# Optimization experiments

Hardware: AMD Instinct MI355X
Metric: run time of the kernel (lower is better)

Reference implementation:

```python
import jax, jax.numpy as jnp
import numpy as np

N, F, D, M, B, K = 100000, 256, 128, 10, 32768, 32


def setup_inputs() -> dict:
    key = jax.random.key(0)
    ks = jax.random.split(key, 14)
    stdv = float(1.0 / np.sqrt(D))
    inp = {
        "feature": jax.random.normal(ks[0], (N, F), jnp.float32),
        "flow_char_adj": jax.random.uniform(ks[1], (M, N), jnp.float32),
        "history": jax.random.randint(ks[2], (B, K), 0, N),
        "item_id": jax.random.randint(ks[3], (B,), 0, N),
        "category_r": jax.random.randint(ks[4], (B,), 0, 2),
        "category_n": jax.random.randint(ks[5], (B,), 0, 2),
        "PA_level": jax.random.randint(ks[6], (B,), 0, M),
        # learned parameters (uniform(-stdv, stdv) as in reset_parameters)
        "weight_emb": jax.random.uniform(ks[7], (F, D), jnp.float32, -stdv, stdv),
        "bias_emb": jax.random.uniform(ks[8], (D,), jnp.float32, -stdv, stdv),
        "weight_character": jax.random.uniform(ks[9], (2 * D, D), jnp.float32, -stdv, stdv),
        "att1_w": jax.random.uniform(ks[10], (D, 1), jnp.float32, -stdv, stdv),
        "att1_b": jax.random.uniform(ks[11], (1,), jnp.float32, -stdv, stdv),
        "linear1_w": jax.random.uniform(ks[12], (2 * D, D), jnp.float32, -stdv, stdv),
        "linear1_b": jax.random.uniform(ks[13], (D,), jnp.float32, -stdv, stdv),
    }
    return inp


def reference(feature, flow_char_adj, weight_emb, bias_emb, weight_character,
              att1_w, att1_b, linear1_w, linear1_b,
              history, item_id, category_r, category_n, PA_level):
    # embedding_encode
    flow_emb = feature @ weight_emb + bias_emb              # [N, D]
    character_emb = flow_char_adj @ flow_emb                # [M, D] (spmm)

    # character_modeling (shared for r and n)
    def char_lat(cat, pa):
        ce = jnp.concatenate([character_emb[cat], character_emb[pa]], axis=1)  # [B, 2D]
        return jax.nn.sigmoid(ce @ weight_character)        # [B, D]

    lat_r = char_lat(category_r, PA_level)
    lat_n = char_lat(category_n, PA_level)

    # attribute_agg: mix flow emb with its 2 category embeddings
    flow_all = (flow_emb + flow_char_adj[:2].T @ character_emb[:2]) * 0.5  # [N, D]

    # Flow_Aggregator: per-node neighbor attention (batched over ragged lists,
    # here padded to fixed degree K)
    neigh = flow_all[history]                                # [B, K, D]
    scores = neigh @ att1_w + att1_b                         # [B, K, 1]
    att = jax.nn.softmax(scores, axis=1)                     # softmax over neighbors
    agg = jnp.sum(att * neigh, axis=1)                       # [B, D]

    # NOTE: in the torch source, self_flow_latent is mutated in-place so
    # self_feats aliases neigh_feats -> both halves of the concat equal agg.
    combined = jnp.concatenate([agg, agg], axis=1)           # [B, 2D]
    out = jax.nn.relu(combined @ linear1_w + linear1_b)      # [B, D] (dropout p=0)

    pred_r = jnp.sum(lat_r * out, axis=1)                    # [B]
    pred_n = jnp.sum(lat_n * out, axis=1)                    # [B]
    return pred_r, pred_n
```

## Files before the change

### kernel.cpp

```cpp
#include <hip/hip_runtime.h>
#include <cmath>

#define NN 100000
#define FF 256
#define DDIM 128
#define MM 10
#define BB 32768
#define KK 32
#define NB1 1563

#define OFF_Q    0
#define OFF_CE   100096
#define OFF_LAT  101376
#define OFF_WPP  103936
#define OFF_CE01 120320
#define OFF_CS   120576
#define OFF_AGG  120592
#define OFF_FE8  4314896
#define OFF_WF   7514896

typedef __attribute__((ext_vector_type(8))) short bf16x8;
typedef __attribute__((ext_vector_type(4))) float floatx4;
typedef __attribute__((ext_vector_type(2))) float floatx2;

__device__ __forceinline__ unsigned short f2bf(float x) {
  union { float f; unsigned u; } v; v.f = x;
  unsigned r = v.u + 0x7FFFu + ((v.u >> 16) & 1u);
  return (unsigned short)(r >> 16);
}
__device__ __forceinline__ float bf2f(unsigned short h) {
  union { float f; unsigned u; } v; v.u = ((unsigned)h) << 16;
  return v.f;
}

__global__ __launch_bounds__(256) void k0_wprep(const float* __restrict__ wemb,
                                                short* __restrict__ wf)
{
  const int t = blockIdx.x * 256 + threadIdx.x;
  const int kk = t >> 9, rem = t & 511;
  const int ct = rem >> 6, l = rem & 63;
  const int n = ct * 16 + (l & 15);
  const int kbase = kk * 32 + (l >> 4) * 8;
  short hi[8], lo[8];
#pragma unroll
  for (int j = 0; j < 8; j++) {
    const float x = wemb[(kbase + j) * 128 + n];
    const unsigned short h = f2bf(x);
    hi[j] = (short)h;
    lo[j] = (short)f2bf(x - bf2f(h));
  }
  const int off = ((kk * 8 + ct) * 64 + l) * 8;
  *reinterpret_cast<int4*>(&wf[off])         = *reinterpret_cast<int4*>(hi);
  *reinterpret_cast<int4*>(&wf[32768 + off]) = *reinterpret_cast<int4*>(lo);
}

__device__ __forceinline__ void split8v(float4 a, float4 b,
                                        bf16x8& hi8, bf16x8& lo8)
{
  const float xs[8] = {a.x, a.y, a.z, a.w, b.x, b.y, b.z, b.w};
  short h[8], l[8];
#pragma unroll
  for (int j = 0; j < 8; j++) {
    const unsigned short hh = f2bf(xs[j]);
    h[j] = (short)hh;
    l[j] = (short)f2bf(xs[j] - bf2f(hh));
  }
  hi8 = *reinterpret_cast<bf16x8*>(h);
  lo8 = *reinterpret_cast<bf16x8*>(l);
}

__global__ __launch_bounds__(128) void k1_fused(const float* __restrict__ feat,
    const short* __restrict__ wf, const float* __restrict__ bemb,
    const float* __restrict__ attw, const float* __restrict__ adj,
    float* __restrict__ q, unsigned char* __restrict__ fe8,
    float* __restrict__ ce)
{
  __shared__ __align__(16) unsigned char ldst[128 * 144];
  const int tid = threadIdx.x;
  const int wv = tid >> 6, l = tid & 63;
  const int lane16 = l & 15, quad = l >> 4;
  const int rowbase = blockIdx.x * 64 + wv * 32;

  floatx4 acc[2][8];
#pragma unroll
  for (int rt = 0; rt < 2; rt++)
#pragma unroll
    for (int ct = 0; ct < 8; ct++) acc[rt][ct] = floatx4{0.f, 0.f, 0.f, 0.f};

  int r0 = rowbase + lane16;      if (r0 > NN - 1) r0 = NN - 1;
  int r1 = rowbase + 16 + lane16; if (r1 > NN - 1) r1 = NN - 1;
  const float* pa0 = &feat[(size_t)r0 * 256 + quad * 8];
  const float* pa1 = &feat[(size_t)r1 * 256 + quad * 8];

  float4 A0a = *reinterpret_cast<const float4*>(pa0);
  float4 A0b = *reinterpret_cast<const float4*>(pa0 + 4);
  float4 A1a = *reinterpret_cast<const float4*>(pa1);
  float4 A1b = *reinterpret_cast<const float4*>(pa1 + 4);

  for (int kk = 0; kk < 8; kk++) {
    float4 N0a, N0b, N1a, N1b;
    if (kk < 7) {
      N0a = *reinterpret_cast<const float4*>(pa0 + (kk + 1) * 32);
      N0b = *reinterpret_cast<const float4*>(pa0 + (kk + 1) * 32 + 4);
      N1a = *reinterpret_cast<const float4*>(pa1 + (kk + 1) * 32);
      N1b = *reinterpret_cast<const float4*>(pa1 + (kk + 1) * 32 + 4);
    }
    bf16x8 a0h, a0l, a1h, a1l;
    split8v(A0a, A0b, a0h, a0l);
    split8v(A1a, A1b, a1h, a1l);
    const short* wb = &wf[kk * 4096 + l * 8];
#pragma unroll
    for (int ct = 0; ct < 8; ct++) {
      const bf16x8 bh = *reinterpret_cast<const bf16x8*>(&wb[ct * 512]);
      const bf16x8 bl = *reinterpret_cast<const bf16x8*>(&wb[32768 + ct * 512]);
      acc[0][ct] = __builtin_amdgcn_mfma_f32_16x16x32_bf16(a0h, bh, acc[0][ct], 0, 0, 0);
      acc[1][ct] = __builtin_amdgcn_mfma_f32_16x16x32_bf16(a1h, bh, acc[1][ct], 0, 0, 0);
      acc[0][ct] = __builtin_amdgcn_mfma_f32_16x16x32_bf16(a0l, bh, acc[0][ct], 0, 0, 0);
      acc[1][ct] = __builtin_amdgcn_mfma_f32_16x16x32_bf16(a1l, bh, acc[1][ct], 0, 0, 0);
      acc[0][ct] = __builtin_amdgcn_mfma_f32_16x16x32_bf16(a0h, bl, acc[0][ct], 0, 0, 0);
      acc[1][ct] = __builtin_amdgcn_mfma_f32_16x16x32_bf16(a1h, bl, acc[1][ct], 0, 0, 0);
    }
    A0a = N0a; A0b = N0b; A1a = N1a; A1b = N1b;
  }

  float bembv[8], attwv[8];
#pragma unroll
  for (int ct = 0; ct < 8; ct++) {
    bembv[ct] = bemb[ct * 16 + lane16];
    attwv[ct] = attw[ct * 16 + lane16];
  }
#pragma unroll
  for (int rt = 0; rt < 2; rt++) {
#pragma unroll
    for (int reg = 0; reg < 4; reg++) {
      const int rloc = (rt * 16 + quad * 4 + reg) + wv * 32;
      const int r = blockIdx.x * 64 + rloc;
      float v[8]; float qp = 0.f;
#pragma unroll
      for (int ct = 0; ct < 8; ct++) {
        v[ct] = acc[rt][ct][reg] + bembv[ct];
        qp = fmaf(v[ct], attwv[ct], qp);
      }
      acc[rt][0][reg] = v[0]; acc[rt][1][reg] = v[1]; acc[rt][2][reg] = v[2]; acc[rt][3][reg] = v[3];
      acc[rt][4][reg] = v[4]; acc[rt][5][reg] = v[5]; acc[rt][6][reg] = v[6]; acc[rt][7][reg] = v[7];
      qp += __shfl_xor(qp, 1, 16);
      qp += __shfl_xor(qp, 2, 16);
      qp += __shfl_xor(qp, 4, 16);
      qp += __shfl_xor(qp, 8, 16);
      if (r < NN) {
        unsigned u0 = __builtin_amdgcn_cvt_pk_fp8_f32(v[0], v[1], 0, false);
        u0 = __builtin_amdgcn_cvt_pk_fp8_f32(v[2], v[3], u0, true);
        unsigned u1 = __builtin_amdgcn_cvt_pk_fp8_f32(v[4], v[5], 0, false);
        u1 = __builtin_amdgcn_cvt_pk_fp8_f32(v[6], v[7], u1, true);
        *reinterpret_cast<uint2*>(&fe8[(size_t)r * 128 + lane16 * 8]) = make_uint2(u0, u1);
        if (lane16 == 0) q[r] = 0.5f * qp;
      }
    }
  }
#pragma unroll
  for (int rt = 0; rt < 2; rt++) {
#pragma unroll
    for (int rp = 0; rp < 2; rp++) {
      const int rloc = wv * 32 + rt * 16 + quad * 4 + rp * 2;
      const int g0 = blockIdx.x * 64 + rloc;
#pragma unroll
      for (int ct = 0; ct < 8; ct++) {
        const unsigned short h0 = (g0     < NN) ? f2bf(acc[rt][ct][rp * 2])     : (unsigned short)0;
        const unsigned short h1 = (g0 + 1 < NN) ? f2bf(acc[rt][ct][rp * 2 + 1]) : (unsigned short)0;
        const unsigned pk = (unsigned)h0 | ((unsigned)h1 << 16);
        *reinterpret_cast<unsigned*>(&ldst[(ct * 16 + lane16) * 144 + rloc * 2]) = pk;
      }
    }
  }
  __syncthreads();

  floatx4 cacc[4];
#pragma unroll
  for (int tt = 0; tt < 4; tt++) cacc[tt] = floatx4{0.f, 0.f, 0.f, 0.f};
  const int mclamp = (lane16 < 10) ? lane16 : 9;
  for (int kc = 0; kc < 2; kc++) {
    int n0 = blockIdx.x * 64 + kc * 32 + quad * 8;
    if (n0 > NN - 8) n0 = NN - 8;
    const float4 f0 = *reinterpret_cast<const float4*>(&adj[(size_t)mclamp * NN + n0]);
    const float4 f1 = *reinterpret_cast<const float4*>(&adj[(size_t)mclamp * NN + n0 + 4]);
    short af[8];
    af[0] = (short)f2bf(f0.x); af[1] = (short)f2bf(f0.y);
    af[2] = (short)f2bf(f0.z); af[3] = (short)f2bf(f0.w);
    af[4] = (short)f2bf(f1.x); af[5] = (short)f2bf(f1.y);
    af[6] = (short)f2bf(f1.z); af[7] = (short)f2bf(f1.w);
    const bf16x8 afr = *reinterpret_cast<bf16x8*>(af);
#pragma unroll
    for (int tt = 0; tt < 4; tt++) {
      const int col = (wv * 4 + tt) * 16 + lane16;
      const bf16x8 bfr = *reinterpret_cast<const bf16x8*>(
          &ldst[col * 144 + (kc * 32 + quad * 8) * 2]);
      cacc[tt] = __builtin_amdgcn_mfma_f32_16x16x32_bf16(afr, bfr, cacc[tt], 0, 0, 0);
    }
  }
#pragma unroll
  for (int tt = 0; tt < 4; tt++) {
#pragma unroll
    for (int reg = 0; reg < 4; reg++) {
      const int m = quad * 4 + reg;
      if (m < 10)
        atomicAdd(&ce[m * 128 + (wv * 4 + tt) * 16 + lane16], cacc[tt][reg]);
    }
  }
}

template<int NCHUNK>
__device__ __forceinline__ void gemm_main(const float* __restrict__ A, int lda, int rowclamp,
                                          const float* __restrict__ W,
                                          int rowbase, int tid,
                                          float (*AT)[128], float (*WT)[128],
                                          float (&acc)[8][8])
{
  const int a_r  = tid >> 4;
  const int a_f4 = tid & 15;
  const int w_k  = tid >> 5;
  const int w_f4 = tid & 31;
  const int tx = tid & 15, ty = tid >> 4;

#pragma unroll
  for (int i = 0; i < 8; i++)
#pragma unroll
    for (int j = 0; j < 8; j++) acc[i][j] = 0.f;

  for (int cc = 0; cc < NCHUNK; cc++) {
    const int kc = cc * 64;
#pragma unroll
    for (int i = 0; i < 8; i++) {
      int r = a_r + 16 * i;
      int gr = rowbase + r; gr = (gr > rowclamp) ? rowclamp : gr;
      const float4 v = *reinterpret_cast<const float4*>(&A[gr * lda + kc + a_f4 * 4]);
      const int X = a_f4 * 4;
      const int col = r ^ X;
      AT[X + 0][col] = v.x;
      AT[X + 1][col] = v.y;
      AT[X + 2][col] = v.z;
      AT[X + 3][col] = v.w;
    }
#pragma unroll
    for (int i = 0; i < 8; i++) {
      const int k = w_k + 8 * i;
      *reinterpret_cast<float4*>(&WT[k][w_f4 * 4]) =
          *reinterpret_cast<const float4*>(&W[(kc + k) * 128 + w_f4 * 4]);
    }
    __syncthreads();
#pragma unroll 8
    for (int k = 0; k < 64; k++) {
      const int X = k & 60;
      const float4 va0 = *reinterpret_cast<const float4*>(&AT[k][(ty * 4) ^ X]);
      const float4 va1 = *reinterpret_cast<const float4*>(&AT[k][((ty * 4) ^ X) + 64]);
      const float4 vb0 = *reinterpret_cast<const float4*>(&WT[k][tx * 4]);
      const float4 vb1 = *reinterpret_cast<const float4*>(&WT[k][tx * 4 + 64]);
      const float a[8] = {va0.x, va0.y, va0.z, va0.w, va1.x, va1.y, va1.z, va1.w};
      const float b[8] = {vb0.x, vb0.y, vb0.z, vb0.w, vb1.x, vb1.y, vb1.z, vb1.w};
#pragma unroll
      for (int i = 0; i < 8; i++)
#pragma unroll
        for (int j = 0; j < 8; j++)
          acc[i][j] = fmaf(a[i], b[j], acc[i][j]);
    }
    __syncthreads();
  }
}

__global__ __launch_bounds__(128) void k3_prep(const float* __restrict__ ce,
    const float* __restrict__ wchar, const float* __restrict__ attw,
    const float* __restrict__ l1w,
    float* __restrict__ latTab, float* __restrict__ Wpp,
    float* __restrict__ ce01p, float* __restrict__ cs)
{
  const int blk = blockIdx.x, tid = threadIdx.x;
  __shared__ float cec[128], cep[128];
  if (blk < 20) {
    const int c = blk / 10, p = blk % 10;
    cec[tid] = ce[c * 128 + tid];
    cep[tid] = ce[p * 128 + tid];
    __syncthreads();
    float s = 0.f;
#pragma unroll 4
    for (int j = 0; j < 128; j++) {
      s = fmaf(cec[j], wchar[j * 128 + tid], s);
      s = fmaf(cep[j], wchar[(128 + j) * 128 + tid], s);
    }
    latTab[blk * 128 + tid] = 1.f / (1.f + expf(-s));
  } else {
    const float s0 = ce[tid];
    const float s1 = ce[128 + tid];
    const int pidx = (tid & 15) * 8 + (tid >> 4);
    ce01p[pidx] = s0;
    ce01p[128 + pidx] = s1;
    cec[tid] = s0 * attw[tid];
    cep[tid] = s1 * attw[tid];
    __syncthreads();
    if (tid < 64) {
      float p0 = cec[tid] + cec[tid + 64];
      float p1 = cep[tid] + cep[tid + 64];
#pragma unroll
      for (int off = 32; off >= 1; off >>= 1) {
        p0 += __shfl_xor(p0, off);
        p1 += __shfl_xor(p1, off);
      }
      if (tid == 0) { cs[0] = 0.5f * p0; cs[1] = 0.5f * p1; }
    }
    for (int i = 0; i < 128; i++) {
      const int pi = (i & 15) * 8 + (i >> 4);
      Wpp[pi * 128 + tid] = l1w[i * 128 + tid] + l1w[16384 + i * 128 + tid];
    }
  }
}

__global__ __launch_bounds__(256) void k4a_attn(const unsigned char* __restrict__ fe8,
    const float* __restrict__ q, const float* __restrict__ adj,
    const int* __restrict__ history, const float* __restrict__ cs,
    const float* __restrict__ attb_p, const float* __restrict__ ce01p,
    float* __restrict__ agg)
{
  const int tid = threadIdx.x;
  const int lane = tid & 63;
  const int wv = tid >> 6;
  const int half = lane >> 5;
  const int t = lane & 31;
  const int b = blockIdx.x * 8 + wv * 2 + half;

  const int n_my = history[b * 32 + t];
  const float a0 = adj[n_my];
  const float a1 = adj[NN + n_my];
  const float sc = q[n_my] + a0 * cs[0] + a1 * cs[1] + attb_p[0];
  float m = sc;
#pragma unroll
  for (int off = 16; off >= 1; off >>= 1) m = fmaxf(m, __shfl_xor(m, off, 32));
  const float e = expf(sc - m);
  float sum = e;
#pragma unroll
  for (int off = 16; off >= 1; off >>= 1) sum += __shfl_xor(sum, off, 32);
  const float att = e / sum;
  float p0 = att * a0, p1 = att * a1;
#pragma unroll
  for (int off = 16; off >= 1; off >>= 1) {
    p0 += __shfl_xor(p0, off, 32);
    p1 += __shfl_xor(p1, off, 32);
  }

  float4 acc = make_float4(0.f, 0.f, 0.f, 0.f);
#pragma unroll
  for (int k = 0; k < 32; k++) {
    const int nk = __shfl(n_my, k, 32);
    const float ak = __shfl(att, k, 32);
    const unsigned u = *reinterpret_cast<const unsigned*>(&fe8[(size_t)nk * 128 + t * 4]);
    const floatx2 lo = __builtin_amdgcn_cvt_pk_f32_fp8(u, false);
    const floatx2 hi = __builtin_amdgcn_cvt_pk_f32_fp8(u, true);
    acc.x = fmaf(ak, lo[0], acc.x);
    acc.y = fmaf(ak, lo[1], acc.y);
    acc.z = fmaf(ak, hi[0], acc.z);
    acc.w = fmaf(ak, hi[1], acc.w);
  }
  const int col = t * 4;
  const float4 c0 = *reinterpret_cast<const float4*>(&ce01p[col]);
  const float4 c1 = *reinterpret_cast<const float4*>(&ce01p[128 + col]);
  float4 o;
  o.x = 0.5f * (acc.x + p0 * c0.x + p1 * c1.x);
  o.y = 0.5f * (acc.y + p0 * c0.y + p1 * c1.y);
  o.z = 0.5f * (acc.z + p0 * c0.z + p1 * c1.z);
  o.w = 0.5f * (acc.w + p0 * c0.w + p1 * c1.w);
  *reinterpret_cast<float4*>(&agg[(size_t)b * 128 + col]) = o;
}

__global__ __launch_bounds__(256) void k4b_out(const float* __restrict__ agg,
    const float* __restrict__ Wpp, const float* __restrict__ l1b,
    const float* __restrict__ latTab,
    const int* __restrict__ cr, const int* __restrict__ cn, const int* __restrict__ pa,
    float* __restrict__ out)
{
  __shared__ __align__(16) float AT[64][128];
  __shared__ __align__(16) float WT[64][128];
  const int tid = threadIdx.x;
  const int tx = tid & 15, ty = tid >> 4;
  const int rowbase = blockIdx.x * 128;
  float acc[8][8];
  gemm_main<2>(agg, 128, BB - 1, Wpp, rowbase, tid, AT, WT, acc);

  int* latIdx = reinterpret_cast<int*>(&AT[0][0]);
  if (tid < 128) {
    const int b = rowbase + tid;
    latIdx[tid * 2]     = (cr[b] * 10 + pa[b]) * 128;
    latIdx[tid * 2 + 1] = (cn[b] * 10 + pa[b]) * 128;
  }
  __syncthreads();

  const float4 b0 = *reinterpret_cast<const float4*>(&l1b[tx * 4]);
  const float4 b1 = *reinterpret_cast<const float4*>(&l1b[tx * 4 + 64]);
  const float bb[8] = {b0.x, b0.y, b0.z, b0.w, b1.x, b1.y, b1.z, b1.w};
#pragma unroll
  for (int i = 0; i < 8; i++) {
    const int r = (i < 4) ? (ty * 4 + i) : (64 + ty * 4 + (i - 4));
    const int b = rowbase + r;
    const int ir = latIdx[r * 2], in_ = latIdx[r * 2 + 1];
    const float4 lr0 = *reinterpret_cast<const float4*>(&latTab[ir + tx * 4]);
    const float4 lr1 = *reinterpret_cast<const float4*>(&latTab[ir + tx * 4 + 64]);
    const float4 ln0 = *reinterpret_cast<const float4*>(&latTab[in_ + tx * 4]);
    const float4 ln1 = *reinterpret_cast<const float4*>(&latTab[in_ + tx * 4 + 64]);
    const float lr[8] = {lr0.x, lr0.y, lr0.z, lr0.w, lr1.x, lr1.y, lr1.z, lr1.w};
    const float ln[8] = {ln0.x, ln0.y, ln0.z, ln0.w, ln1.x, ln1.y, ln1.z, ln1.w};
    float pr = 0.f, pn = 0.f;
#pragma unroll
    for (int j = 0; j < 8; j++) {
      const float v = fmaxf(acc[i][j] + bb[j], 0.f);
      pr = fmaf(v, lr[j], pr);
      pn = fmaf(v, ln[j], pn);
    }
    pr += __shfl_down(pr, 8, 16); pr += __shfl_down(pr, 4, 16);
    pr += __shfl_down(pr, 2, 16); pr += __shfl_down(pr, 1, 16);
    pn += __shfl_down(pn, 8, 16); pn += __shfl_down(pn, 4, 16);
    pn += __shfl_down(pn, 2, 16); pn += __shfl_down(pn, 1, 16);
    if (tx == 0) { out[b] = pr; out[BB + b] = pn; }
  }
}

extern "C" void kernel_launch(void* const* d_in, const int* in_sizes, int n_in,
                              void* d_out, int out_size, void* d_ws, size_t ws_size,
                              hipStream_t stream) {
  const float* feat  = (const float*)d_in[0];
  const float* adj   = (const float*)d_in[1];
  const int*   hist  = (const int*)d_in[2];
  const int*   cr    = (const int*)d_in[4];
  const int*   cn    = (const int*)d_in[5];
  const int*   pa    = (const int*)d_in[6];
  const float* wemb  = (const float*)d_in[7];
  const float* bemb  = (const float*)d_in[8];
  const float* wchar = (const float*)d_in[9];
  const float* attw  = (const float*)d_in[10];
  const float* attb  = (const float*)d_in[11];
  const float* l1w   = (const float*)d_in[12];
  const float* l1b   = (const float*)d_in[13];
  float* out = (float*)d_out;
  float* ws  = (float*)d_ws;

  float* q     = ws + OFF_Q;
  float* ce    = ws + OFF_CE;
  float* lat   = ws + OFF_LAT;
  float* Wpp   = ws + OFF_WPP;
  float* ce01p = ws + OFF_CE01;
  float* cs    = ws + OFF_CS;
  float* agg   = ws + OFF_AGG;
  unsigned char* fe8 = (unsigned char*)(ws + OFF_FE8);
  short* wf    = (short*)(ws + OFF_WF);

  hipMemsetAsync(ce, 0, 1280 * sizeof(float), stream);
  k0_wprep<<<16, 256, 0, stream>>>(wemb, wf);
  k1_fused<<<NB1, 128, 0, stream>>>(feat, wf, bemb, attw, adj, q, fe8, ce);
  k3_prep<<<21, 128, 0, stream>>>(ce, wchar, attw, l1w, lat, Wpp, ce01p, cs);
  k4a_attn<<<4096, 256, 0, stream>>>(fe8, q, adj, hist, cs, attb, ce01p, agg);
  k4b_out<<<256, 256, 0, stream>>>(agg, Wpp, l1b, lat, cr, cn, pa, out);
}
```

Baseline: 311.3 us.

## Drop split-bf16 precision, use MFMA for output GEMM, replicate atomic accumulators

The feature-embedding GEMM now uses single bf16 operands instead of the hi/lo split, cutting MFMA work to a third. The final linear layer moves from an FP32 LDS-tiled GEMM to bf16 MFMA, with a bf16 aggregate buffer and a pre-summed, pre-permuted weight built in the prep kernel. k1 blocks are widened to 128 rows with a two-deep feature prefetch, and character-embedding atomics are spread over 64 replicas and summed by a new small reduction kernel. The cost is lower numerical accuracy from bf16 rounding, which may push results past the tolerance.

```diff
diff --git a/kernel.cpp b/kernel.cpp
--- a/kernel.cpp
+++ b/kernel.cpp
@@ -7,17 +7,19 @@
 #define MM 10
 #define BB 32768
 #define KK 32
-#define NB1 1563
-
-#define OFF_Q    0
-#define OFF_CE   100096
-#define OFF_LAT  101376
-#define OFF_WPP  103936
-#define OFF_CE01 120320
-#define OFF_CS   120576
-#define OFF_AGG  120592
-#define OFF_FE8  4314896
-#define OFF_WF   7514896
+#define NB1 782
+#define NREP 64
+
+#define OFF_Q     0
+#define OFF_CEREP 100096
+#define OFF_CE    182016
+#define OFF_LAT   183296
+#define OFF_CE01  185856
+#define OFF_CS    186112
+#define OFF_AGGB  186128
+#define OFF_FE8   2283280
+#define OFF_WF    5483280
+#define OFF_WPF   5499664
 
 typedef __attribute__((ext_vector_type(8))) short bf16x8;
 typedef __attribute__((ext_vector_type(4))) float floatx4;
@@ -28,58 +30,58 @@
   unsigned r = v.u + 0x7FFFu + ((v.u >> 16) & 1u);
   return (unsigned short)(r >> 16);
 }
-__device__ __forceinline__ float bf2f(unsigned short h) {
-  union { float f; unsigned u; } v; v.u = ((unsigned)h) << 16;
-  return v.f;
+
+__device__ __forceinline__ bf16x8 cvt8(float4 a, float4 b) {
+  short h[8];
+  h[0] = (short)f2bf(a.x); h[1] = (short)f2bf(a.y);
+  h[2] = (short)f2bf(a.z); h[3] = (short)f2bf(a.w);
+  h[4] = (short)f2bf(b.x); h[5] = (short)f2bf(b.y);
+  h[6] = (short)f2bf(b.z); h[7] = (short)f2bf(b.w);
+  return *reinterpret_cast<bf16x8*>(h);
 }
 
 __global__ __launch_bounds__(256) void k0_wprep(const float* __restrict__ wemb,
-                                                short* __restrict__ wf)
+                                                const float* __restrict__ l1w,
+                                                short* __restrict__ wf,
+                                                short* __restrict__ wpf)
 {
   const int t = blockIdx.x * 256 + threadIdx.x;
-  const int kk = t >> 9, rem = t & 511;
-  const int ct = rem >> 6, l = rem & 63;
-  const int n = ct * 16 + (l & 15);
-  const int kbase = kk * 32 + (l >> 4) * 8;
-  short hi[8], lo[8];
-#pragma unroll
-  for (int j = 0; j < 8; j++) {
-    const float x = wemb[(kbase + j) * 128 + n];
-    const unsigned short h = f2bf(x);
-    hi[j] = (short)h;
-    lo[j] = (short)f2bf(x - bf2f(h));
-  }
-  const int off = ((kk * 8 + ct) * 64 + l) * 8;
-  *reinterpret_cast<int4*>(&wf[off])         = *reinterpret_cast<int4*>(hi);
-  *reinterpret_cast<int4*>(&wf[32768 + off]) = *reinterpret_cast<int4*>(lo);
-}
-
-__device__ __forceinline__ void split8v(float4 a, float4 b,
-                                        bf16x8& hi8, bf16x8& lo8)
-{
-  const float xs[8] = {a.x, a.y, a.z, a.w, b.x, b.y, b.z, b.w};
-  short h[8], l[8];
-#pragma unroll
-  for (int j = 0; j < 8; j++) {
-    const unsigned short hh = f2bf(xs[j]);
-    h[j] = (short)hh;
-    l[j] = (short)f2bf(xs[j] - bf2f(hh));
-  }
-  hi8 = *reinterpret_cast<bf16x8*>(h);
-  lo8 = *reinterpret_cast<bf16x8*>(l);
-}
-
-__global__ __launch_bounds__(128) void k1_fused(const float* __restrict__ feat,
+  if (t < 4096) {
+    const int kk = t >> 9, rem = t & 511;
+    const int ct = rem >> 6, l = rem & 63;
+    const int n = ct * 16 + (l & 15);
+    const int kbase = kk * 32 + (l >> 4) * 8;
+    short hi[8];
+#pragma unroll
+    for (int j = 0; j < 8; j++) hi[j] = (short)f2bf(wemb[(kbase + j) * 128 + n]);
+    *reinterpret_cast<int4*>(&wf[((kk * 8 + ct) * 64 + l) * 8]) = *reinterpret_cast<int4*>(hi);
+  } else {
+    const int t2 = t - 4096;
+    const int kk = t2 >> 9, rem = t2 & 511;
+    const int ct = rem >> 6, l = rem & 63;
+    const int n = ct * 16 + (l & 15);
+    short h[8];
+#pragma unroll
+    for (int j = 0; j < 8; j++) {
+      const int kp = kk * 32 + (l >> 4) * 8 + j;
+      const int i = ((kp & 7) << 4) | (kp >> 3);
+      h[j] = (short)f2bf(l1w[i * 128 + n] + l1w[(128 + i) * 128 + n]);
+    }
+    *reinterpret_cast<int4*>(&wpf[((kk * 8 + ct) * 64 + l) * 8]) = *reinterpret_cast<int4*>(h);
+  }
+}
+
+__global__ __launch_bounds__(256) void k1_fused(const float* __restrict__ feat,
     const short* __restrict__ wf, const float* __restrict__ bemb,
     const float* __restrict__ attw, const float* __restrict__ adj,
     float* __restrict__ q, unsigned char* __restrict__ fe8,
-    float* __restrict__ ce)
-{
-  __shared__ __align__(16) unsigned char ldst[128 * 144];
+    float* __restrict__ cerep)
+{
+  __shared__ __align__(16) unsigned char ldst[128 * 272];
   const int tid = threadIdx.x;
   const int wv = tid >> 6, l = tid & 63;
   const int lane16 = l & 15, quad = l >> 4;
-  const int rowbase = blockIdx.x * 64 + wv * 32;
+  const int rowbase = blockIdx.x * 128 + wv * 32;
 
   floatx4 acc[2][8];
 #pragma unroll
@@ -92,35 +94,33 @@
   const float* pa0 = &feat[(size_t)r0 * 256 + quad * 8];
   const float* pa1 = &feat[(size_t)r1 * 256 + quad * 8];
 
-  float4 A0a = *reinterpret_cast<const float4*>(pa0);
-  float4 A0b = *reinterpret_cast<const float4*>(pa0 + 4);
-  float4 A1a = *reinterpret_cast<const float4*>(pa1);
-  float4 A1b = *reinterpret_cast<const float4*>(pa1 + 4);
+  float4 pb[2][2][2];
+  pb[0][0][0] = *reinterpret_cast<const float4*>(pa0);
+  pb[0][0][1] = *reinterpret_cast<const float4*>(pa0 + 4);
+  pb[0][1][0] = *reinterpret_cast<const float4*>(pa1);
+  pb[0][1][1] = *reinterpret_cast<const float4*>(pa1 + 4);
+  pb[1][0][0] = *reinterpret_cast<const float4*>(pa0 + 32);
+  pb[1][0][1] = *reinterpret_cast<const float4*>(pa0 + 36);
+  pb[1][1][0] = *reinterpret_cast<const float4*>(pa1 + 32);
+  pb[1][1][1] = *reinterpret_cast<const float4*>(pa1 + 36);
 
   for (int kk = 0; kk < 8; kk++) {
-    float4 N0a, N0b, N1a, N1b;
-    if (kk < 7) {
-      N0a = *reinterpret_cast<const float4*>(pa0 + (kk + 1) * 32);
-      N0b = *reinterpret_cast<const float4*>(pa0 + (kk + 1) * 32 + 4);
-      N1a = *reinterpret_cast<const float4*>(pa1 + (kk + 1) * 32);
-      N1b = *reinterpret_cast<const float4*>(pa1 + (kk + 1) * 32 + 4);
-    }
-    bf16x8 a0h, a0l, a1h, a1l;
-    split8v(A0a, A0b, a0h, a0l);
-    split8v(A1a, A1b, a1h, a1l);
+    const int par = kk & 1;
+    const bf16x8 a0 = cvt8(pb[par][0][0], pb[par][0][1]);
+    const bf16x8 a1 = cvt8(pb[par][1][0], pb[par][1][1]);
+    if (kk < 6) {
+      pb[par][0][0] = *reinterpret_cast<const float4*>(pa0 + (kk + 2) * 32);
+      pb[par][0][1] = *reinterpret_cast<const float4*>(pa0 + (kk + 2) * 32 + 4);
+      pb[par][1][0] = *reinterpret_cast<const float4*>(pa1 + (kk + 2) * 32);
+      pb[par][1][1] = *reinterpret_cast<const float4*>(pa1 + (kk + 2) * 32 + 4);
+    }
     const short* wb = &wf[kk * 4096 + l * 8];
 #pragma unroll
     for (int ct = 0; ct < 8; ct++) {
       const bf16x8 bh = *reinterpret_cast<const bf16x8*>(&wb[ct * 512]);
-      const bf16x8 bl = *reinterpret_cast<const bf16x8*>(&wb[32768 + ct * 512]);
-      acc[0][ct] = __builtin_amdgcn_mfma_f32_16x16x32_bf16(a0h, bh, acc[0][ct], 0, 0, 0);
-      acc[1][ct] = __builtin_amdgcn_mfma_f32_16x16x32_bf16(a1h, bh, acc[1][ct], 0, 0, 0);
-      acc[0][ct] = __builtin_amdgcn_mfma_f32_16x16x32_bf16(a0l, bh, acc[0][ct], 0, 0, 0);
-      acc[1][ct] = __builtin_amdgcn_mfma_f32_16x16x32_bf16(a1l, bh, acc[1][ct], 0, 0, 0);
-      acc[0][ct] = __builtin_amdgcn_mfma_f32_16x16x32_bf16(a0h, bl, acc[0][ct], 0, 0, 0);
-      acc[1][ct] = __builtin_amdgcn_mfma_f32_16x16x32_bf16(a1h, bl, acc[1][ct], 0, 0, 0);
-    }
-    A0a = N0a; A0b = N0b; A1a = N1a; A1b = N1b;
+      acc[0][ct] = __builtin_amdgcn_mfma_f32_16x16x32_bf16(a0, bh, acc[0][ct], 0, 0, 0);
+      acc[1][ct] = __builtin_amdgcn_mfma_f32_16x16x32_bf16(a1, bh, acc[1][ct], 0, 0, 0);
+    }
   }
 
   float bembv[8], attwv[8];
@@ -133,8 +133,7 @@
   for (int rt = 0; rt < 2; rt++) {
 #pragma unroll
     for (int reg = 0; reg < 4; reg++) {
-      const int rloc = (rt * 16 + quad * 4 + reg) + wv * 32;
-      const int r = blockIdx.x * 64 + rloc;
+      const int r = rowbase + rt * 16 + quad * 4 + reg;
       float v[8]; float qp = 0.f;
 #pragma unroll
       for (int ct = 0; ct < 8; ct++) {
@@ -162,115 +161,64 @@
 #pragma unroll
     for (int rp = 0; rp < 2; rp++) {
       const int rloc = wv * 32 + rt * 16 + quad * 4 + rp * 2;
-      const int g0 = blockIdx.x * 64 + rloc;
+      const int g0 = blockIdx.x * 128 + rloc;
 #pragma unroll
       for (int ct = 0; ct < 8; ct++) {
         const unsigned short h0 = (g0     < NN) ? f2bf(acc[rt][ct][rp * 2])     : (unsigned short)0;
         const unsigned short h1 = (g0 + 1 < NN) ? f2bf(acc[rt][ct][rp * 2 + 1]) : (unsigned short)0;
         const unsigned pk = (unsigned)h0 | ((unsigned)h1 << 16);
-        *reinterpret_cast<unsigned*>(&ldst[(ct * 16 + lane16) * 144 + rloc * 2]) = pk;
+        *reinterpret_cast<unsigned*>(&ldst[(ct * 16 + lane16) * 272 + rloc * 2]) = pk;
       }
     }
   }
   __syncthreads();
 
-  floatx4 cacc[4];
-#pragma unroll
-  for (int tt = 0; tt < 4; tt++) cacc[tt] = floatx4{0.f, 0.f, 0.f, 0.f};
+  floatx4 cacc[2];
+  cacc[0] = floatx4{0.f, 0.f, 0.f, 0.f};
+  cacc[1] = floatx4{0.f, 0.f, 0.f, 0.f};
   const int mclamp = (lane16 < 10) ? lane16 : 9;
-  for (int kc = 0; kc < 2; kc++) {
-    int n0 = blockIdx.x * 64 + kc * 32 + quad * 8;
+#pragma unroll
+  for (int kc = 0; kc < 4; kc++) {
+    int n0 = blockIdx.x * 128 + kc * 32 + quad * 8;
     if (n0 > NN - 8) n0 = NN - 8;
     const float4 f0 = *reinterpret_cast<const float4*>(&adj[(size_t)mclamp * NN + n0]);
     const float4 f1 = *reinterpret_cast<const float4*>(&adj[(size_t)mclamp * NN + n0 + 4]);
-    short af[8];
-    af[0] = (short)f2bf(f0.x); af[1] = (short)f2bf(f0.y);
-    af[2] = (short)f2bf(f0.z); af[3] = (short)f2bf(f0.w);
-    af[4] = (short)f2bf(f1.x); af[5] = (short)f2bf(f1.y);
-    af[6] = (short)f2bf(f1.z); af[7] = (short)f2bf(f1.w);
-    const bf16x8 afr = *reinterpret_cast<bf16x8*>(af);
-#pragma unroll
-    for (int tt = 0; tt < 4; tt++) {
-      const int col = (wv * 4 + tt) * 16 + lane16;
+    const bf16x8 afr = cvt8(f0, f1);
+#pragma unroll
+    for (int tt = 0; tt < 2; tt++) {
+      const int col = (wv * 2 + tt) * 16 + lane16;
       const bf16x8 bfr = *reinterpret_cast<const bf16x8*>(
-          &ldst[col * 144 + (kc * 32 + quad * 8) * 2]);
+          &ldst[col * 272 + (kc * 32 + quad * 8) * 2]);
       cacc[tt] = __builtin_amdgcn_mfma_f32_16x16x32_bf16(afr, bfr, cacc[tt], 0, 0, 0);
     }
   }
-#pragma unroll
-  for (int tt = 0; tt < 4; tt++) {
+  float* myrep = &cerep[(blockIdx.x & (NREP - 1)) * 1280];
+#pragma unroll
+  for (int tt = 0; tt < 2; tt++) {
 #pragma unroll
     for (int reg = 0; reg < 4; reg++) {
       const int m = quad * 4 + reg;
       if (m < 10)
-        atomicAdd(&ce[m * 128 + (wv * 4 + tt) * 16 + lane16], cacc[tt][reg]);
-    }
-  }
-}
-
-template<int NCHUNK>
-__device__ __forceinline__ void gemm_main(const float* __restrict__ A, int lda, int rowclamp,
-                                          const float* __restrict__ W,
-                                          int rowbase, int tid,
-                                          float (*AT)[128], float (*WT)[128],
-                                          float (&acc)[8][8])
-{
-  const int a_r  = tid >> 4;
-  const int a_f4 = tid & 15;
-  const int w_k  = tid >> 5;
-  const int w_f4 = tid & 31;
-  const int tx = tid & 15, ty = tid >> 4;
-
-#pragma unroll
-  for (int i = 0; i < 8; i++)
-#pragma unroll
-    for (int j = 0; j < 8; j++) acc[i][j] = 0.f;
-
-  for (int cc = 0; cc < NCHUNK; cc++) {
-    const int kc = cc * 64;
-#pragma unroll
-    for (int i = 0; i < 8; i++) {
-      int r = a_r + 16 * i;
-      int gr = rowbase + r; gr = (gr > rowclamp) ? rowclamp : gr;
-      const float4 v = *reinterpret_cast<const float4*>(&A[gr * lda + kc + a_f4 * 4]);
-      const int X = a_f4 * 4;
-      const int col = r ^ X;
-      AT[X + 0][col] = v.x;
-      AT[X + 1][col] = v.y;
-      AT[X + 2][col] = v.z;
-      AT[X + 3][col] = v.w;
-    }
-#pragma unroll
-    for (int i = 0; i < 8; i++) {
-      const int k = w_k + 8 * i;
-      *reinterpret_cast<float4*>(&WT[k][w_f4 * 4]) =
-          *reinterpret_cast<const float4*>(&W[(kc + k) * 128 + w_f4 * 4]);
-    }
-    __syncthreads();
+        atomicAdd(&myrep[m * 128 + (wv * 2 + tt) * 16 + lane16], cacc[tt][reg]);
+    }
+  }
+}
+
+__global__ __launch_bounds__(256) void k3r_reduce(const float* __restrict__ cerep,
+                                                  float* __restrict__ ce)
+{
+  const int o = blockIdx.x * 256 + threadIdx.x;
+  if (o < 1280) {
+    float s = 0.f;
 #pragma unroll 8
-    for (int k = 0; k < 64; k++) {
-      const int X = k & 60;
-      const float4 va0 = *reinterpret_cast<const float4*>(&AT[k][(ty * 4) ^ X]);
-      const float4 va1 = *reinterpret_cast<const float4*>(&AT[k][((ty * 4) ^ X) + 64]);
-      const float4 vb0 = *reinterpret_cast<const float4*>(&WT[k][tx * 4]);
-      const float4 vb1 = *reinterpret_cast<const float4*>(&WT[k][tx * 4 + 64]);
-      const float a[8] = {va0.x, va0.y, va0.z, va0.w, va1.x, va1.y, va1.z, va1.w};
-      const float b[8] = {vb0.x, vb0.y, vb0.z, vb0.w, vb1.x, vb1.y, vb1.z, vb1.w};
-#pragma unroll
-      for (int i = 0; i < 8; i++)
-#pragma unroll
-        for (int j = 0; j < 8; j++)
-          acc[i][j] = fmaf(a[i], b[j], acc[i][j]);
-    }
-    __syncthreads();
+    for (int r = 0; r < NREP; r++) s += cerep[r * 1280 + o];
+    ce[o] = s;
   }
 }
 
 __global__ __launch_bounds__(128) void k3_prep(const float* __restrict__ ce,
     const float* __restrict__ wchar, const float* __restrict__ attw,
-    const float* __restrict__ l1w,
-    float* __restrict__ latTab, float* __restrict__ Wpp,
-    float* __restrict__ ce01p, float* __restrict__ cs)
+    float* __restrict__ latTab, float* __restrict__ ce01p, float* __restrict__ cs)
 {
   const int blk = blockIdx.x, tid = threadIdx.x;
   __shared__ float cec[128], cep[128];
@@ -305,10 +253,6 @@
       }
       if (tid == 0) { cs[0] = 0.5f * p0; cs[1] = 0.5f * p1; }
     }
-    for (int i = 0; i < 128; i++) {
-      const int pi = (i & 15) * 8 + (i >> 4);
-      Wpp[pi * 128 + tid] = l1w[i * 128 + tid] + l1w[16384 + i * 128 + tid];
-    }
   }
 }
 
@@ -316,7 +260,7 @@
     const float* __restrict__ q, const float* __restrict__ adj,
     const int* __restrict__ history, const float* __restrict__ cs,
     const float* __restrict__ attb_p, const float* __restrict__ ce01p,
-    float* __restrict__ agg)
+    short* __restrict__ aggb)
 {
   const int tid = threadIdx.x;
   const int lane = tid & 63;
@@ -360,62 +304,70 @@
   const int col = t * 4;
   const float4 c0 = *reinterpret_cast<const float4*>(&ce01p[col]);
   const float4 c1 = *reinterpret_cast<const float4*>(&ce01p[128 + col]);
-  float4 o;
-  o.x = 0.5f * (acc.x + p0 * c0.x + p1 * c1.x);
-  o.y = 0.5f * (acc.y + p0 * c0.y + p1 * c1.y);
-  o.z = 0.5f * (acc.z + p0 * c0.z + p1 * c1.z);
-  o.w = 0.5f * (acc.w + p0 * c0.w + p1 * c1.w);
-  *reinterpret_cast<float4*>(&agg[(size_t)b * 128 + col]) = o;
-}
-
-__global__ __launch_bounds__(256) void k4b_out(const float* __restrict__ agg,
-    const float* __restrict__ Wpp, const float* __restrict__ l1b,
+  const float ox = 0.5f * (acc.x + p0 * c0.x + p1 * c1.x);
+  const float oy = 0.5f * (acc.y + p0 * c0.y + p1 * c1.y);
+  const float oz = 0.5f * (acc.z + p0 * c0.z + p1 * c1.z);
+  const float ow = 0.5f * (acc.w + p0 * c0.w + p1 * c1.w);
+  const unsigned lo_ = (unsigned)f2bf(ox) | ((unsigned)f2bf(oy) << 16);
+  const unsigned hi_ = (unsigned)f2bf(oz) | ((unsigned)f2bf(ow) << 16);
+  *reinterpret_cast<uint2*>(&aggb[(size_t)b * 128 + col]) = make_uint2(lo_, hi_);
+}
+
+__global__ __launch_bounds__(256) void k4b_mfma(const short* __restrict__ aggb,
+    const short* __restrict__ wpf, const float* __restrict__ l1b,
     const float* __restrict__ latTab,
     const int* __restrict__ cr, const int* __restrict__ cn, const int* __restrict__ pa,
     float* __restrict__ out)
 {
-  __shared__ __align__(16) float AT[64][128];
-  __shared__ __align__(16) float WT[64][128];
   const int tid = threadIdx.x;
-  const int tx = tid & 15, ty = tid >> 4;
-  const int rowbase = blockIdx.x * 128;
-  float acc[8][8];
-  gemm_main<2>(agg, 128, BB - 1, Wpp, rowbase, tid, AT, WT, acc);
-
-  int* latIdx = reinterpret_cast<int*>(&AT[0][0]);
-  if (tid < 128) {
-    const int b = rowbase + tid;
-    latIdx[tid * 2]     = (cr[b] * 10 + pa[b]) * 128;
-    latIdx[tid * 2 + 1] = (cn[b] * 10 + pa[b]) * 128;
-  }
-  __syncthreads();
-
-  const float4 b0 = *reinterpret_cast<const float4*>(&l1b[tx * 4]);
-  const float4 b1 = *reinterpret_cast<const float4*>(&l1b[tx * 4 + 64]);
-  const float bb[8] = {b0.x, b0.y, b0.z, b0.w, b1.x, b1.y, b1.z, b1.w};
-#pragma unroll
-  for (int i = 0; i < 8; i++) {
-    const int r = (i < 4) ? (ty * 4 + i) : (64 + ty * 4 + (i - 4));
-    const int b = rowbase + r;
-    const int ir = latIdx[r * 2], in_ = latIdx[r * 2 + 1];
-    const float4 lr0 = *reinterpret_cast<const float4*>(&latTab[ir + tx * 4]);
-    const float4 lr1 = *reinterpret_cast<const float4*>(&latTab[ir + tx * 4 + 64]);
-    const float4 ln0 = *reinterpret_cast<const float4*>(&latTab[in_ + tx * 4]);
-    const float4 ln1 = *reinterpret_cast<const float4*>(&latTab[in_ + tx * 4 + 64]);
-    const float lr[8] = {lr0.x, lr0.y, lr0.z, lr0.w, lr1.x, lr1.y, lr1.z, lr1.w};
-    const float ln[8] = {ln0.x, ln0.y, ln0.z, ln0.w, ln1.x, ln1.y, ln1.z, ln1.w};
-    float pr = 0.f, pn = 0.f;
-#pragma unroll
-    for (int j = 0; j < 8; j++) {
-      const float v = fmaxf(acc[i][j] + bb[j], 0.f);
-      pr = fmaf(v, lr[j], pr);
-      pn = fmaf(v, ln[j], pn);
-    }
-    pr += __shfl_down(pr, 8, 16); pr += __shfl_down(pr, 4, 16);
-    pr += __shfl_down(pr, 2, 16); pr += __shfl_down(pr, 1, 16);
-    pn += __shfl_down(pn, 8, 16); pn += __shfl_down(pn, 4, 16);
-    pn += __shfl_down(pn, 2, 16); pn += __shfl_down(pn, 1, 16);
-    if (tx == 0) { out[b] = pr; out[BB + b] = pn; }
+  const int wv = tid >> 6, l = tid & 63;
+  const int lane16 = l & 15, quad = l >> 4;
+  const int rowbase = blockIdx.x * 128 + wv * 32;
+  const int r0 = rowbase + lane16;
+  const int r1 = r0 + 16;
+
+  floatx4 acc[2][8];
+#pragma unroll
+  for (int rt = 0; rt < 2; rt++)
+#pragma unroll
+    for (int ct = 0; ct < 8; ct++) acc[rt][ct] = floatx4{0.f, 0.f, 0.f, 0.f};
+
+#pragma unroll
+  for (int kk = 0; kk < 4; kk++) {
+    const bf16x8 a0 = *reinterpret_cast<const bf16x8*>(&aggb[(size_t)r0 * 128 + kk * 32 + quad * 8]);
+    const bf16x8 a1 = *reinterpret_cast<const bf16x8*>(&aggb[(size_t)r1 * 128 + kk * 32 + quad * 8]);
+    const short* wb = &wpf[kk * 4096 + l * 8];
+#pragma unroll
+    for (int ct = 0; ct < 8; ct++) {
+      const bf16x8 bh = *reinterpret_cast<const bf16x8*>(&wb[ct * 512]);
+      acc[0][ct] = __builtin_amdgcn_mfma_f32_16x16x32_bf16(a0, bh, acc[0][ct], 0, 0, 0);
+      acc[1][ct] = __builtin_amdgcn_mfma_f32_16x16x32_bf16(a1, bh, acc[1][ct], 0, 0, 0);
+    }
+  }
+
+  float bb[8];
+#pragma unroll
+  for (int ct = 0; ct < 8; ct++) bb[ct] = l1b[ct * 16 + lane16];
+#pragma unroll
+  for (int rt = 0; rt < 2; rt++) {
+#pragma unroll
+    for (int reg = 0; reg < 4; reg++) {
+      const int r = rowbase + rt * 16 + quad * 4 + reg;
+      const int ir  = (cr[r] * 10 + pa[r]) * 128;
+      const int in_ = (cn[r] * 10 + pa[r]) * 128;
+      float pr = 0.f, pn = 0.f;
+#pragma unroll
+      for (int ct = 0; ct < 8; ct++) {
+        const float v = fmaxf(acc[rt][ct][reg] + bb[ct], 0.f);
+        pr = fmaf(v, latTab[ir  + ct * 16 + lane16], pr);
+        pn = fmaf(v, latTab[in_ + ct * 16 + lane16], pn);
+      }
+      pr += __shfl_xor(pr, 1, 16); pr += __shfl_xor(pr, 2, 16);
+      pr += __shfl_xor(pr, 4, 16); pr += __shfl_xor(pr, 8, 16);
+      pn += __shfl_xor(pn, 1, 16); pn += __shfl_xor(pn, 2, 16);
+      pn += __shfl_xor(pn, 4, 16); pn += __shfl_xor(pn, 8, 16);
+      if (lane16 == 0) { out[r] = pr; out[BB + r] = pn; }
+    }
   }
 }
 
@@ -439,19 +391,21 @@
   float* ws  = (float*)d_ws;
 
   float* q     = ws + OFF_Q;
+  float* cerep = ws + OFF_CEREP;
   float* ce    = ws + OFF_CE;
   float* lat   = ws + OFF_LAT;
-  float* Wpp   = ws + OFF_WPP;
   float* ce01p = ws + OFF_CE01;
   float* cs    = ws + OFF_CS;
-  float* agg   = ws + OFF_AGG;
+  short* aggb  = (short*)(ws + OFF_AGGB);
   unsigned char* fe8 = (unsigned char*)(ws + OFF_FE8);
   short* wf    = (short*)(ws + OFF_WF);
-
-  hipMemsetAsync(ce, 0, 1280 * sizeof(float), stream);
-  k0_wprep<<<16, 256, 0, stream>>>(wemb, wf);
-  k1_fused<<<NB1, 128, 0, stream>>>(feat, wf, bemb, attw, adj, q, fe8, ce);
-  k3_prep<<<21, 128, 0, stream>>>(ce, wchar, attw, l1w, lat, Wpp, ce01p, cs);
-  k4a_attn<<<4096, 256, 0, stream>>>(fe8, q, adj, hist, cs, attb, ce01p, agg);
-  k4b_out<<<256, 256, 0, stream>>>(agg, Wpp, l1b, lat, cr, cn, pa, out);
-}
+  short* wpf   = (short*)(ws + OFF_WPF);
+
+  hipMemsetAsync(cerep, 0, NREP * 1280 * sizeof(float), stream);
+  k0_wprep<<<24, 256, 0, stream>>>(wemb, l1w, wf, wpf);
+  k1_fused<<<NB1, 256, 0, stream>>>(feat, wf, bemb, attw, adj, q, fe8, cerep);
+  k3r_reduce<<<5, 256, 0, stream>>>(cerep, ce);
+  k3_prep<<<21, 128, 0, stream>>>(ce, wchar, attw, lat, ce01p, cs);
+  k4a_attn<<<4096, 256, 0, stream>>>(fe8, q, adj, hist, cs, attb, ce01p, aggb);
+  k4b_mfma<<<256, 256, 0, stream>>>(aggb, wpf, l1b, lat, cr, cn, pa, out);
+}
```

After: 275.0 us. -11.6%, faster.
